# Kernel tuning notes

Measured on AMD Instinct MI355X. Metric: run time of the kernel, lower is better.

The kernel has to match this reference:

```python
import jax, jax.numpy as jnp
import numpy as np

QLEN, MLEN, BSZ = 1024, 1024, 4
D_MODEL, N_HEAD, D_HEAD, D_INNER = 1024, 16, 64, 4096
KLEN = QLEN + MLEN  # = rlen
LN_EPS = 1e-5


def setup_inputs() -> dict:
    key = jax.random.key(0)
    ks = jax.random.split(key, 16)
    s = 0.02
    nhd = N_HEAD * D_HEAD
    inp = {
        "dec_inp": jax.random.normal(ks[0], (QLEN, BSZ, D_MODEL), jnp.float32),
        "r": jax.random.normal(ks[1], (KLEN, D_MODEL), jnp.float32),
        "r_w_bias": jax.random.normal(ks[2], (N_HEAD, D_HEAD), jnp.float32) * s,
        "r_r_bias": jax.random.normal(ks[3], (N_HEAD, D_HEAD), jnp.float32) * s,
        "mems": jax.random.normal(ks[4], (MLEN, BSZ, D_MODEL), jnp.float32),
        # causal mask with memory: position j visible to query i iff j <= i + MLEN
        "dec_attn_mask": (jnp.arange(KLEN)[None, :] > (jnp.arange(QLEN)[:, None] + MLEN))[:, :, None],
        # parameters
        "qkv_w": jax.random.normal(ks[5], (D_MODEL, 3 * nhd), jnp.float32) * s,
        "r_w": jax.random.normal(ks[6], (D_MODEL, nhd), jnp.float32) * s,
        "o_w": jax.random.normal(ks[7], (nhd, D_MODEL), jnp.float32) * s,
        "ln1_w": jnp.ones((D_MODEL,), jnp.float32),
        "ln1_b": jnp.zeros((D_MODEL,), jnp.float32),
        "ln2_w": jnp.ones((D_MODEL,), jnp.float32),
        "ln2_b": jnp.zeros((D_MODEL,), jnp.float32),
        "ff_w1": jax.random.normal(ks[8], (D_MODEL, D_INNER), jnp.float32) * s,
        "ff_b1": jnp.zeros((D_INNER,), jnp.float32),
        "ff_w2": jax.random.normal(ks[9], (D_INNER, D_MODEL), jnp.float32) * s,
        "ff_b2": jnp.zeros((D_MODEL,), jnp.float32),
    }
    return inp


def _layer_norm(x, w, b):
    mu = jnp.mean(x, axis=-1, keepdims=True)
    var = jnp.mean(jnp.square(x - mu), axis=-1, keepdims=True)
    return (x - mu) * jax.lax.rsqrt(var + LN_EPS) * w + b


def _rel_shift(x):
    # x: [qlen, rlen, bsz, n_head] -- Transformer-XL pad/reshape shift
    q, rl = x.shape[0], x.shape[1]
    zero_pad = jnp.zeros((q, 1) + x.shape[2:], x.dtype)
    x_padded = jnp.concatenate([zero_pad, x], axis=1)
    x_padded = x_padded.reshape((rl + 1, q) + x.shape[2:])
    return x_padded[1:].reshape(x.shape)


def reference(dec_inp, r, r_w_bias, r_r_bias, mems, dec_attn_mask,
              qkv_w, r_w, o_w, ln1_w, ln1_b, ln2_w, ln2_b,
              ff_w1, ff_b1, ff_w2, ff_b2):
    qlen, bsz = dec_inp.shape[0], dec_inp.shape[1]
    nhd = N_HEAD * D_HEAD
    scale = 1.0 / (D_HEAD ** 0.5)

    cat = jnp.concatenate([mems, dec_inp], axis=0)          # [klen, b, d]
    w_heads = cat @ qkv_w                                   # [klen, b, 3*nhd]
    w_head_q, w_head_k, w_head_v = jnp.split(w_heads, 3, axis=-1)
    w_head_q = w_head_q[-qlen:]                             # [qlen, b, nhd]
    klen = w_head_k.shape[0]

    w_head_q = w_head_q.reshape(qlen, bsz, N_HEAD, D_HEAD)
    w_head_k = w_head_k.reshape(klen, bsz, N_HEAD, D_HEAD)
    w_head_v = w_head_v.reshape(klen, bsz, N_HEAD, D_HEAD)
    r_head_k = (r @ r_w).reshape(-1, N_HEAD, D_HEAD)        # [rlen, n, d]

    AC = jnp.einsum('ibnd,jbnd->ijbn', w_head_q + r_w_bias, w_head_k)
    BD = jnp.einsum('ibnd,jnd->ijbn', w_head_q + r_r_bias, r_head_k)
    BD = _rel_shift(BD)

    attn_score = (AC + BD) * scale                          # [q, k, b, n]
    attn_score = jnp.where(dec_attn_mask[:, :, :, None], -jnp.inf, attn_score)
    attn_prob = jax.nn.softmax(attn_score, axis=1)

    attn_vec = jnp.einsum('ijbn,jbnd->ibnd', attn_prob, w_head_v)
    attn_out = attn_vec.reshape(qlen, bsz, nhd) @ o_w       # [q, b, d]

    output = _layer_norm(dec_inp + attn_out, ln1_w, ln1_b)
    ff = jax.nn.relu(output @ ff_w1 + ff_b1) @ ff_w2 + ff_b2
    return _layer_norm(output + ff, ln2_w, ln2_b)
```

## Files before the change

### kernel.cpp

```cpp
#include <hip/hip_runtime.h>
#include <hip/hip_bf16.h>
#include <math.h>

#define QLEN 1024
#define MLEN 1024
#define BSZ 4
#define KLEN 2048
#define NH 16
#define DH 64
#define DM 1024
#define DI 4096
#define NHD 1024
#define LN_EPS 1e-5f

typedef short bf16x8 __attribute__((ext_vector_type(8)));
typedef float f32x4 __attribute__((ext_vector_type(4)));
typedef unsigned int uint4v __attribute__((ext_vector_type(4)));

__device__ __forceinline__ float bf2f(unsigned short u) {
    union { unsigned u32; float f; } x; x.u32 = ((unsigned)u) << 16; return x.f;
}
__device__ __forceinline__ unsigned short f2bf(float f) {
    __hip_bfloat16 h = __float2bfloat16(f);
    return *(unsigned short*)&h;
}

static const size_t OFF_CATB  = 0;
static const size_t OFF_VTG   = 0;
static const size_t OFF_WHB   = 16777216;
static const size_t OFF_RB    = 67108864;
static const size_t OFF_RHKB  = 71303168;
static const size_t OFF_AVB   = 75497472;
static const size_t OFF_TMP   = 83886080;
static const size_t OFF_LN1F  = 100663296;
static const size_t OFF_LN1B  = 117440512;
static const size_t OFF_FFHB  = 125829120;
static const size_t OFF_QKVWT = 159383552;
static const size_t OFF_RWT   = 165675008;
static const size_t OFF_OWT   = 167772160;
static const size_t OFF_FFW1T = 169869312;
static const size_t OFF_FFW2T = 178257920;
static const size_t OFF_BK    = 186646528;
static const size_t OFF_BR    = 187170816;

__global__ __launch_bounds__(256) void cast_cat(const float* __restrict__ mems,
                                                const float* __restrict__ dec,
                                                unsigned short* __restrict__ out) {
    size_t i8 = ((size_t)blockIdx.x * 256 + threadIdx.x) * 8;
    const size_t half = (size_t)MLEN * BSZ * DM;
    const float* src = (i8 < half) ? (mems + i8) : (dec + (i8 - half));
    float4 v0 = *(const float4*)src;
    float4 v1 = *(const float4*)(src + 4);
    ushort4 o0 = {f2bf(v0.x), f2bf(v0.y), f2bf(v0.z), f2bf(v0.w)};
    ushort4 o1 = {f2bf(v1.x), f2bf(v1.y), f2bf(v1.z), f2bf(v1.w)};
    *(ushort4*)&out[i8] = o0;
    *(ushort4*)&out[i8 + 4] = o1;
}

__global__ __launch_bounds__(256) void cast_f32_bf16(const float* __restrict__ in,
                                                     unsigned short* __restrict__ out) {
    size_t i8 = ((size_t)blockIdx.x * 256 + threadIdx.x) * 8;
    float4 v0 = *(const float4*)(in + i8);
    float4 v1 = *(const float4*)(in + i8 + 4);
    ushort4 o0 = {f2bf(v0.x), f2bf(v0.y), f2bf(v0.z), f2bf(v0.w)};
    ushort4 o1 = {f2bf(v1.x), f2bf(v1.y), f2bf(v1.z), f2bf(v1.w)};
    *(ushort4*)&out[i8] = o0;
    *(ushort4*)&out[i8 + 4] = o1;
}

__global__ __launch_bounds__(256) void transpose_cast(const float* __restrict__ in,
                                                      unsigned short* __restrict__ out,
                                                      int K, int N) {
    __shared__ float tile[32][33];
    const int t = threadIdx.x;
    const int n0 = blockIdx.x * 32;
    const int k0 = blockIdx.y * 32;
    const int r = t >> 3;
    const int c0 = (t & 7) << 2;
    float4 v = *(const float4*)&in[(size_t)(k0 + r) * N + n0 + c0];
    tile[r][c0 + 0] = v.x; tile[r][c0 + 1] = v.y;
    tile[r][c0 + 2] = v.z; tile[r][c0 + 3] = v.w;
    __syncthreads();
    ushort4 o = {f2bf(tile[c0 + 0][r]), f2bf(tile[c0 + 1][r]),
                 f2bf(tile[c0 + 2][r]), f2bf(tile[c0 + 3][r])};
    *(ushort4*)&out[(size_t)(n0 + r) * K + k0 + c0] = o;
}

__global__ __launch_bounds__(256) void gemm_bf16(const unsigned short* __restrict__ A,
                                                 const unsigned short* __restrict__ Bt,
                                                 const float* __restrict__ bias,
                                                 void* __restrict__ C,
                                                 int M, int N, int K, int flags) {
    __shared__ __align__(16) unsigned short As[128 * 64];
    __shared__ __align__(16) unsigned short Bs[128 * 64];

    const int tid = threadIdx.x;
    const int w = tid >> 6, l = tid & 63;
    const int wr = w >> 1, wc = w & 1;
    const int row0 = blockIdx.y * 128;
    const int col0 = blockIdx.x * 128;

    f32x4 acc[4][4] = {};

    uint4v ra[4], rb[4];
    {
#pragma unroll
        for (int q = 0; q < 4; ++q) {
            int f = q * 256 + tid, r = f >> 3, c = f & 7;
            ra[q] = *(const uint4v*)&A[(size_t)(row0 + r) * K + c * 8];
            rb[q] = *(const uint4v*)&Bt[(size_t)(col0 + r) * K + c * 8];
        }
    }

    const int nt = K >> 6;
    for (int kt = 0; kt < nt; ++kt) {
        __syncthreads();
#pragma unroll
        for (int q = 0; q < 4; ++q) {
            int f = q * 256 + tid, r = f >> 3, c = f & 7;
            int sw = (c ^ (r & 7)) << 3;
            *(uint4v*)&As[r * 64 + sw] = ra[q];
            *(uint4v*)&Bs[r * 64 + sw] = rb[q];
        }
        __syncthreads();
        if (kt + 1 < nt) {
            const int k0 = (kt + 1) << 6;
#pragma unroll
            for (int q = 0; q < 4; ++q) {
                int f = q * 256 + tid, r = f >> 3, c = f & 7;
                ra[q] = *(const uint4v*)&A[(size_t)(row0 + r) * K + k0 + c * 8];
                rb[q] = *(const uint4v*)&Bt[(size_t)(col0 + r) * K + k0 + c * 8];
            }
        }
#pragma unroll
        for (int ks = 0; ks < 2; ++ks) {
            bf16x8 a[4], bfr[4];
#pragma unroll
            for (int m = 0; m < 4; ++m) {
                int arow = wr * 64 + m * 16 + (l & 15);
                int chunk = (ks * 4 + (l >> 4)) ^ (arow & 7);
                a[m] = *(const bf16x8*)&As[arow * 64 + chunk * 8];
            }
#pragma unroll
            for (int n = 0; n < 4; ++n) {
                int brow = wc * 64 + n * 16 + (l & 15);
                int chunk = (ks * 4 + (l >> 4)) ^ (brow & 7);
                bfr[n] = *(const bf16x8*)&Bs[brow * 64 + chunk * 8];
            }
#pragma unroll
            for (int m = 0; m < 4; ++m)
#pragma unroll
                for (int n = 0; n < 4; ++n)
                    acc[m][n] = __builtin_amdgcn_mfma_f32_16x16x32_bf16(a[m], bfr[n], acc[m][n], 0, 0, 0);
        }
    }

#pragma unroll
    for (int n = 0; n < 4; ++n) {
        const int ccol = col0 + wc * 64 + n * 16 + (l & 15);
        const float bv = (flags & 1) ? bias[ccol] : 0.0f;
#pragma unroll
        for (int m = 0; m < 4; ++m) {
            const int crow0 = row0 + wr * 64 + m * 16 + ((l >> 4) << 2);
#pragma unroll
            for (int reg = 0; reg < 4; ++reg) {
                float v = acc[m][n][reg] + bv;
                if (flags & 2) v = fmaxf(v, 0.0f);
                if (flags & 4)
                    ((unsigned short*)C)[(size_t)(crow0 + reg) * N + ccol] = f2bf(v);
                else
                    ((float*)C)[(size_t)(crow0 + reg) * N + ccol] = v;
            }
        }
    }
}

__global__ __launch_bounds__(256) void vtrans(const unsigned short* __restrict__ whb,
                                              unsigned short* __restrict__ vtg) {
    __shared__ unsigned short tile[64][72];
    const int bn = blockIdx.y;
    const int b = bn >> 4, n = bn & 15, nb = n * 64;
    const int jt0 = blockIdx.x * 64;
    const int tid = threadIdx.x;
#pragma unroll
    for (int g = 0; g < 2; ++g) {
        int f = g * 256 + tid;
        int key = f >> 3, c = f & 7;
        uint4v v = *(const uint4v*)&whb[((size_t)(jt0 + key) * 4 + b) * 3072 + 2048 + nb + c * 8];
        *(uint4v*)&tile[key][c * 8] = v;
    }
    __syncthreads();
#pragma unroll
    for (int g = 0; g < 2; ++g) {
        int f = g * 256 + tid;
        int d = f >> 3, ck = f & 7;
        unsigned short tmp[8];
#pragma unroll
        for (int e = 0; e < 8; ++e) tmp[e] = tile[ck * 8 + e][d];
        *(uint4v*)&vtg[(size_t)bn * 131072 + (size_t)d * 2048 + jt0 + ck * 8] = *(uint4v*)tmp;
    }
}

__global__ __launch_bounds__(256) void bias_kernel(const unsigned short* __restrict__ whb,
                                                   const unsigned short* __restrict__ rhkb,
                                                   const float* __restrict__ r_w_bias,
                                                   const float* __restrict__ r_r_bias,
                                                   float* __restrict__ bias_k,
                                                   float* __restrict__ bias_r) {
    int id = blockIdx.x * 256 + threadIdx.x;
    if (id < 64 * 2048) {
        int bn = id >> 11, j = id & 2047;
        int b = bn >> 4, n = bn & 15;
        const unsigned short* kp = &whb[((size_t)j * 4 + b) * 3072 + 1024 + n * 64];
        const float* wb = &r_w_bias[n * 64];
        float acc = 0.f;
#pragma unroll
        for (int d = 0; d < 64; ++d) acc += wb[d] * bf2f(kp[d]);
        bias_k[id] = acc * 0.125f;
    } else {
        int id2 = id - 64 * 2048;
        if (id2 < 16 * 2048) {
            int n = id2 >> 11, rel = id2 & 2047;
            const unsigned short* rp = &rhkb[(size_t)rel * 1024 + n * 64];
            const float* rb = &r_r_bias[n * 64];
            float acc = 0.f;
#pragma unroll
            for (int d = 0; d < 64; ++d) acc += rb[d] * bf2f(rp[d]);
            bias_r[id2] = acc * 0.125f;
        }
    }
}

__global__ __launch_bounds__(512) void flash_attn_mfma(const unsigned short* __restrict__ whb,
                                                       const unsigned short* __restrict__ rhkb,
                                                       const unsigned short* __restrict__ vtg,
                                                       const float* __restrict__ bias_k,
                                                       const float* __restrict__ bias_r,
                                                       unsigned short* __restrict__ avb) {
    const int bid = blockIdx.x;
    const int bn = bid >> 3;
    const int z = bid & 7;
    const int bx = (z & 1) ? (z >> 1) : 7 - (z >> 1);
    const int b = bn >> 4, n = bn & 15, nb = n * 64;
    const int i0 = bx << 7;
    const int tid = threadIdx.x;
    const int wq = tid >> 6;
    const int lane = tid & 63;
    const int rg = lane >> 4;
    const int lc = lane & 15;

    __shared__ __align__(16) unsigned short Ks[4096];
    __shared__ __align__(16) unsigned short Rs[16384];
    __shared__ __align__(16) unsigned short Vt[4096];
    __shared__ __align__(16) unsigned short WS[8][1600];

    bf16x8 qf[2];
    {
        const int qrow = MLEN + i0 + wq * 16 + lc;
        const unsigned short* qp = whb + ((size_t)qrow * 4 + b) * 3072 + nb + rg * 8;
        bf16x8 q0 = *(const bf16x8*)(qp);
        bf16x8 q1 = *(const bf16x8*)(qp + 32);
#pragma unroll
        for (int e = 0; e < 8; ++e) {
            unsigned short u0 = (unsigned short)q0[e];
            unsigned short u1 = (unsigned short)q1[e];
            qf[0][e] = (short)(((u0 & 0x7F80) > 0x0180) ? (unsigned short)(u0 - 0x0180)
                                                        : (unsigned short)(u0 & 0x8000));
            qf[1][e] = (short)(((u1 & 0x7F80) > 0x0180) ? (unsigned short)(u1 - 0x0180)
                                                        : (unsigned short)(u1 & 0x8000));
        }
    }

    f32x4 Oacc[4] = {};
    float mrun[4] = {-INFINITY, -INFINITY, -INFINITY, -INFINITY};
    float lrun[4] = {0.f, 0.f, 0.f, 0.f};

    const int ntiles = 2 * bx + 18;
    const int wbase_off = 112 - 16 * wq;

    const int srow = tid >> 3;
    const int sc = tid & 7;

    uint4v pk, pv, pr3[3];
    {
        pk = *(const uint4v*)&whb[((size_t)srow * 4 + b) * 3072 + 1024 + nb + sc * 8];
        pv = *(const uint4v*)&vtg[(size_t)bn * 131072 + (size_t)srow * 2048 + sc * 8];
        const int relbase0 = 896 - i0;
#pragma unroll
        for (int p = 0; p < 3; ++p) {
            const int a = relbase0 + p * 64 + srow;
            pr3[p] = *(const uint4v*)&rhkb[(size_t)a * 1024 + nb + sc * 8];
        }
    }

    for (int kt = 0; kt < ntiles; ++kt) {
        const int jt0 = kt << 6;
        const int relbase = jt0 - i0 + 896;
        __syncthreads();

        *(uint4v*)&Ks[srow * 64 + ((sc ^ (srow & 7)) << 3)] = pk;
        *(uint4v*)&Vt[srow * 64 + ((sc ^ (srow & 7)) << 3)] = pv;
        if (kt == 0) {
#pragma unroll
            for (int p = 0; p < 3; ++p) {
                const int a = relbase + p * 64 + srow;
                const int dst = ((a >> 6) & 3) * 4096 + (a & 63) * 64 + ((sc ^ (a & 7)) << 3);
                *(uint4v*)&Rs[dst] = pr3[p];
            }
        } else {
            const int a = relbase + 128 + srow;
            const int dst = ((a >> 6) & 3) * 4096 + (a & 63) * 64 + ((sc ^ (a & 7)) << 3);
            *(uint4v*)&Rs[dst] = pr3[0];
        }
        if (kt + 1 < ntiles) {
            const int jn = jt0 + 64;
            pk = *(const uint4v*)&whb[((size_t)(jn + srow) * 4 + b) * 3072 + 1024 + nb + sc * 8];
            pv = *(const uint4v*)&vtg[(size_t)bn * 131072 + (size_t)srow * 2048 + jn + sc * 8];
            int a = relbase + 192 + srow;
            if (a > 2047) a = 2047;
            pr3[0] = *(const uint4v*)&rhkb[(size_t)a * 1024 + nb + sc * 8];
        }
        __syncthreads();

        f32x4 Sacc[4];
        __builtin_amdgcn_s_setprio(1);
#pragma unroll
        for (int nf = 0; nf < 4; ++nf) {
            const int key = nf * 16 + lc;
            const int c7 = key & 7;
            const bf16x8 kf0 = *(const bf16x8*)&Ks[key * 64 + ((rg ^ c7) << 3)];
            const bf16x8 kf1 = *(const bf16x8*)&Ks[key * 64 + (((4 + rg) ^ c7) << 3)];
            f32x4 zz = {0.f, 0.f, 0.f, 0.f};
            zz = __builtin_amdgcn_mfma_f32_16x16x32_bf16(qf[0], kf0, zz, 0, 0, 0);
            Sacc[nf] = __builtin_amdgcn_mfma_f32_16x16x32_bf16(qf[1], kf1, zz, 0, 0, 0);
        }
        __builtin_amdgcn_s_setprio(0);

        unsigned short* bdt = &WS[wq][0];
        const int wbase = relbase + wbase_off;
#pragma unroll
        for (int e5 = 0; e5 < 5; ++e5) {
            const int a = wbase + e5 * 16 + lc;
            const int rbase = ((a >> 6) & 3) * 4096 + (a & 63) * 64;
            const int c7 = a & 7;
            const bf16x8 rf0 = *(const bf16x8*)&Rs[rbase + ((rg ^ c7) << 3)];
            const bf16x8 rf1 = *(const bf16x8*)&Rs[rbase + (((4 + rg) ^ c7) << 3)];
            f32x4 bd = {0.f, 0.f, 0.f, 0.f};
            bd = __builtin_amdgcn_mfma_f32_16x16x32_bf16(qf[0], rf0, bd, 0, 0, 0);
            bd = __builtin_amdgcn_mfma_f32_16x16x32_bf16(qf[1], rf1, bd, 0, 0, 0);
            const int aa = a > 2047 ? 2047 : a;
            const float brv = bias_r[n * 2048 + aa];
            const int bb = e5 * 16 + lc;
            ushort4 p4 = {f2bf(bd[0] + brv), f2bf(bd[1] + brv),
                          f2bf(bd[2] + brv), f2bf(bd[3] + brv)};
            *(ushort4*)&bdt[bb * 20 + rg * 4] = p4;
        }

        float sv[4][4];
        float tmax[4] = {-INFINITY, -INFINITY, -INFINITY, -INFINITY};
#pragma unroll
        for (int nf = 0; nf < 4; ++nf) {
            const int jl = nf * 16 + lc;
            const float bkv = bias_k[(size_t)bn * 2048 + jt0 + jl];
            const int wbb = wbase + 15 + jl;
#pragma unroll
            for (int r = 0; r < 4; ++r) {
                const int qr = rg * 4 + r;
                const int bb = 15 + jl - qr;
                float s = Sacc[nf][r] + bkv + bf2f(bdt[bb * 20 + qr]);
                s = (wbb - qr <= 2047) ? s : -INFINITY;
                sv[nf][r] = s;
                tmax[r] = fmaxf(tmax[r], s);
            }
        }
        float ef[4];
#pragma unroll
        for (int r = 0; r < 4; ++r) {
            float tm = tmax[r];
            tm = fmaxf(tm, __shfl_xor(tm, 1));
            tm = fmaxf(tm, __shfl_xor(tm, 2));
            tm = fmaxf(tm, __shfl_xor(tm, 4));
            tm = fmaxf(tm, __shfl_xor(tm, 8));
            const float mn = fmaxf(mrun[r], tm);
            ef[r] = __expf(mrun[r] - mn);
            mrun[r] = mn;
        }
        float rsum[4] = {0.f, 0.f, 0.f, 0.f};
#pragma unroll
        for (int nf = 0; nf < 4; ++nf) {
            const int jl = nf * 16 + lc;
#pragma unroll
            for (int r = 0; r < 4; ++r) {
                const int qr = rg * 4 + r;
                const float p = __expf(sv[nf][r] - mrun[r]);
                rsum[r] += p;
                bdt[qr * 64 + (((jl >> 3) ^ (qr & 7)) << 3) + (jl & 7)] = f2bf(p);
            }
        }
#pragma unroll
        for (int r = 0; r < 4; ++r) {
            float rs = rsum[r];
            rs += __shfl_xor(rs, 1);
            rs += __shfl_xor(rs, 2);
            rs += __shfl_xor(rs, 4);
            rs += __shfl_xor(rs, 8);
            lrun[r] = lrun[r] * ef[r] + rs;
        }
#pragma unroll
        for (int nf = 0; nf < 4; ++nf)
#pragma unroll
            for (int r = 0; r < 4; ++r) Oacc[nf][r] *= ef[r];

        {
            const int c7 = lc & 7;
            const bf16x8 pf0 = *(const bf16x8*)&bdt[lc * 64 + ((rg ^ c7) << 3)];
            const bf16x8 pf1 = *(const bf16x8*)&bdt[lc * 64 + (((4 + rg) ^ c7) << 3)];
            __builtin_amdgcn_s_setprio(1);
#pragma unroll
            for (int nf = 0; nf < 4; ++nf) {
                const int d = nf * 16 + lc;
                const int d7 = d & 7;
                const bf16x8 vf0 = *(const bf16x8*)&Vt[d * 64 + ((rg ^ d7) << 3)];
                const bf16x8 vf1 = *(const bf16x8*)&Vt[d * 64 + (((4 + rg) ^ d7) << 3)];
                Oacc[nf] = __builtin_amdgcn_mfma_f32_16x16x32_bf16(pf0, vf0, Oacc[nf], 0, 0, 0);
                Oacc[nf] = __builtin_amdgcn_mfma_f32_16x16x32_bf16(pf1, vf1, Oacc[nf], 0, 0, 0);
            }
            __builtin_amdgcn_s_setprio(0);
        }
    }

    float inv[4];
#pragma unroll
    for (int r = 0; r < 4; ++r) inv[r] = 1.0f / lrun[r];
#pragma unroll
    for (int nf = 0; nf < 4; ++nf) {
        const int d = nf * 16 + lc;
#pragma unroll
        for (int r = 0; r < 4; ++r) {
            const int iq = i0 + wq * 16 + rg * 4 + r;
            avb[((size_t)iq * 4 + b) * 1024 + nb + d] = f2bf(Oacc[nf][r] * inv[r]);
        }
    }
}

__global__ __launch_bounds__(256) void add_ln_kernel(const float* __restrict__ a,
                                                     const float* __restrict__ b,
                                                     const float* __restrict__ w,
                                                     const float* __restrict__ bias,
                                                     float* __restrict__ out,
                                                     unsigned short* __restrict__ out_bf) {
    const int row = blockIdx.x;
    const int t = threadIdx.x;
    __shared__ float xs[DM];
    __shared__ float red[256];

    const float* ar = a + (size_t)row * DM;
    const float* br = b + (size_t)row * DM;

    float lsum = 0.f;
#pragma unroll
    for (int c = t; c < DM; c += 256) {
        float v = ar[c] + br[c];
        xs[c] = v;
        lsum += v;
    }
    red[t] = lsum;
    __syncthreads();
    for (int off = 128; off > 0; off >>= 1) {
        if (t < off) red[t] += red[t + off];
        __syncthreads();
    }
    const float mu = red[0] * (1.0f / DM);
    __syncthreads();

    float lvar = 0.f;
#pragma unroll
    for (int c = t; c < DM; c += 256) {
        float dv = xs[c] - mu;
        lvar += dv * dv;
    }
    red[t] = lvar;
    __syncthreads();
    for (int off = 128; off > 0; off >>= 1) {
        if (t < off) red[t] += red[t + off];
        __syncthreads();
    }
    const float rstd = rsqrtf(red[0] * (1.0f / DM) + LN_EPS);
    __syncthreads();

    float* orow = out + (size_t)row * DM;
#pragma unroll
    for (int c = t; c < DM; c += 256) {
        float v = (xs[c] - mu) * rstd * w[c] + bias[c];
        orow[c] = v;
        if (out_bf) out_bf[(size_t)row * DM + c] = f2bf(v);
    }
}

extern "C" void kernel_launch(void* const* d_in, const int* in_sizes, int n_in,
                              void* d_out, int out_size, void* d_ws, size_t ws_size,
                              hipStream_t stream) {
    const float* dec_inp  = (const float*)d_in[0];
    const float* r        = (const float*)d_in[1];
    const float* r_w_bias = (const float*)d_in[2];
    const float* r_r_bias = (const float*)d_in[3];
    const float* mems     = (const float*)d_in[4];
    const float* qkv_w    = (const float*)d_in[6];
    const float* r_w      = (const float*)d_in[7];
    const float* o_w      = (const float*)d_in[8];
    const float* ln1_w    = (const float*)d_in[9];
    const float* ln1_b    = (const float*)d_in[10];
    const float* ln2_w    = (const float*)d_in[11];
    const float* ln2_b    = (const float*)d_in[12];
    const float* ff_w1    = (const float*)d_in[13];
    const float* ff_b1    = (const float*)d_in[14];
    const float* ff_w2    = (const float*)d_in[15];
    const float* ff_b2    = (const float*)d_in[16];
    float* out = (float*)d_out;
    char* ws = (char*)d_ws;

    unsigned short* catb  = (unsigned short*)(ws + OFF_CATB);
    unsigned short* vtg   = (unsigned short*)(ws + OFF_VTG);
    unsigned short* whb   = (unsigned short*)(ws + OFF_WHB);
    unsigned short* rb    = (unsigned short*)(ws + OFF_RB);
    unsigned short* rhkb  = (unsigned short*)(ws + OFF_RHKB);
    unsigned short* avb   = (unsigned short*)(ws + OFF_AVB);
    float*          tmp   = (float*)(ws + OFF_TMP);
    float*          ln1f  = (float*)(ws + OFF_LN1F);
    unsigned short* ln1b  = (unsigned short*)(ws + OFF_LN1B);
    unsigned short* ffhb  = (unsigned short*)(ws + OFF_FFHB);
    unsigned short* qkvwT = (unsigned short*)(ws + OFF_QKVWT);
    unsigned short* rwT   = (unsigned short*)(ws + OFF_RWT);
    unsigned short* owT   = (unsigned short*)(ws + OFF_OWT);
    unsigned short* ffw1T = (unsigned short*)(ws + OFF_FFW1T);
    unsigned short* ffw2T = (unsigned short*)(ws + OFF_FFW2T);
    float*          bk    = (float*)(ws + OFF_BK);
    float*          brr   = (float*)(ws + OFF_BR);

    cast_cat<<<dim3(4096), 256, 0, stream>>>(mems, dec_inp, catb);
    cast_f32_bf16<<<dim3(1024), 256, 0, stream>>>(r, rb);
    transpose_cast<<<dim3(96, 32), 256, 0, stream>>>(qkv_w, qkvwT, 1024, 3072);
    transpose_cast<<<dim3(32, 32), 256, 0, stream>>>(r_w, rwT, 1024, 1024);
    transpose_cast<<<dim3(32, 32), 256, 0, stream>>>(o_w, owT, 1024, 1024);
    transpose_cast<<<dim3(128, 32), 256, 0, stream>>>(ff_w1, ffw1T, 1024, 4096);
    transpose_cast<<<dim3(32, 128), 256, 0, stream>>>(ff_w2, ffw2T, 4096, 1024);

    gemm_bf16<<<dim3(24, 64), 256, 0, stream>>>(catb, qkvwT, nullptr, whb,
                                                KLEN * BSZ, 3 * NHD, DM, 4);
    gemm_bf16<<<dim3(8, 16), 256, 0, stream>>>(rb, rwT, nullptr, rhkb,
                                               KLEN, NHD, DM, 4);

    vtrans<<<dim3(32, 64), 256, 0, stream>>>(whb, vtg);
    bias_kernel<<<dim3(640), 256, 0, stream>>>(whb, rhkb, r_w_bias, r_r_bias, bk, brr);

    flash_attn_mfma<<<dim3(512), 512, 0, stream>>>(
        whb, rhkb, vtg, bk, brr, avb);

    gemm_bf16<<<dim3(8, 32), 256, 0, stream>>>(avb, owT, nullptr, tmp,
                                               QLEN * BSZ, DM, NHD, 0);
    add_ln_kernel<<<dim3(QLEN * BSZ), 256, 0, stream>>>(
        dec_inp, tmp, ln1_w, ln1_b, ln1f, ln1b);
    gemm_bf16<<<dim3(32, 32), 256, 0, stream>>>(ln1b, ffw1T, ff_b1, ffhb,
                                                QLEN * BSZ, DI, DM, 1 | 2 | 4);
    gemm_bf16<<<dim3(8, 32), 256, 0, stream>>>(ffhb, ffw2T, ff_b2, tmp,
                                               QLEN * BSZ, DM, DI, 1);
    add_ln_kernel<<<dim3(QLEN * BSZ), 256, 0, stream>>>(
        ln1f, tmp, ln2_w, ln2_b, out, nullptr);
}
```

Measured before the change: 447.0 us.

## Fuse weight transposes and compute rel-shift BD via lane shuffles in registers

Merges the five weight transpose-cast launches into one kernel that picks its matrix by block index, which removes launch overhead. In the attention kernel the relative-shift BD term is no longer written to a per-wave LDS staging buffer in bf16 and read back. It is now computed per 16-key chunk and realigned with __shfl across lanes, keeping the value in fp32 and shrinking shared memory. It also skips the mask compare on tiles that cannot hit the boundary and skips the O-accumulator rescale when no row max changed, at the cost of extra shuffles and a wave vote.

After: 444.6 us. Within noise of the previous version (-0.5%).

```diff
diff --git a/kernel.cpp b/kernel.cpp
--- a/kernel.cpp
+++ b/kernel.cpp
@@ -68,13 +68,24 @@
     *(ushort4*)&out[i8 + 4] = o1;
 }
 
-__global__ __launch_bounds__(256) void transpose_cast(const float* __restrict__ in,
-                                                      unsigned short* __restrict__ out,
-                                                      int K, int N) {
+__global__ __launch_bounds__(256) void transpose_cast_all(
+        const float* __restrict__ qkv_w, const float* __restrict__ r_w,
+        const float* __restrict__ o_w,  const float* __restrict__ ff_w1,
+        const float* __restrict__ ff_w2,
+        unsigned short* __restrict__ qkvwT, unsigned short* __restrict__ rwT,
+        unsigned short* __restrict__ owT, unsigned short* __restrict__ ffw1T,
+        unsigned short* __restrict__ ffw2T) {
     __shared__ float tile[32][33];
+    const int bid = blockIdx.x;
+    const float* in; unsigned short* out; int K, N, nx, lid;
+    if (bid < 3072)      { in = qkv_w; out = qkvwT; K = 1024; N = 3072; nx = 96;  lid = bid; }
+    else if (bid < 4096) { in = r_w;   out = rwT;   K = 1024; N = 1024; nx = 32;  lid = bid - 3072; }
+    else if (bid < 5120) { in = o_w;   out = owT;   K = 1024; N = 1024; nx = 32;  lid = bid - 4096; }
+    else if (bid < 9216) { in = ff_w1; out = ffw1T; K = 1024; N = 4096; nx = 128; lid = bid - 5120; }
+    else                 { in = ff_w2; out = ffw2T; K = 4096; N = 1024; nx = 32;  lid = bid - 9216; }
+    const int n0 = (lid % nx) * 32;
+    const int k0 = (lid / nx) * 32;
     const int t = threadIdx.x;
-    const int n0 = blockIdx.x * 32;
-    const int k0 = blockIdx.y * 32;
     const int r = t >> 3;
     const int c0 = (t & 7) << 2;
     float4 v = *(const float4*)&in[(size_t)(k0 + r) * N + n0 + c0];
@@ -252,7 +263,7 @@
     __shared__ __align__(16) unsigned short Ks[4096];
     __shared__ __align__(16) unsigned short Rs[16384];
     __shared__ __align__(16) unsigned short Vt[4096];
-    __shared__ __align__(16) unsigned short WS[8][1600];
+    __shared__ __align__(16) unsigned short Ps[8][1024];
 
     bf16x8 qf[2];
     {
@@ -280,6 +291,15 @@
 
     const int srow = tid >> 3;
     const int sc = tid & 7;
+
+    int srcl[4];
+    bool hi5[4];
+#pragma unroll
+    for (int r = 0; r < 4; ++r) {
+        const int qr = rg * 4 + r;
+        srcl[r] = (rg << 4) | ((15 + lc - qr) & 15);
+        hi5[r] = (lc > qr);
+    }
 
     uint4v pk, pv, pr3[3];
     {
@@ -336,11 +356,14 @@
         }
         __builtin_amdgcn_s_setprio(0);
 
-        unsigned short* bdt = &WS[wq][0];
         const int wbase = relbase + wbase_off;
-#pragma unroll
-        for (int e5 = 0; e5 < 5; ++e5) {
-            const int a = wbase + e5 * 16 + lc;
+        const bool needmask = (wbase + 78 > 2047);
+        float sv[4][4];
+        float tmax[4] = {-INFINITY, -INFINITY, -INFINITY, -INFINITY};
+
+        f32x4 bdpA;
+        {
+            const int a = wbase + lc;
             const int rbase = ((a >> 6) & 3) * 4096 + (a & 63) * 64;
             const int c7 = a & 7;
             const bf16x8 rf0 = *(const bf16x8*)&Rs[rbase + ((rg ^ c7) << 3)];
@@ -350,29 +373,44 @@
             bd = __builtin_amdgcn_mfma_f32_16x16x32_bf16(qf[1], rf1, bd, 0, 0, 0);
             const int aa = a > 2047 ? 2047 : a;
             const float brv = bias_r[n * 2048 + aa];
-            const int bb = e5 * 16 + lc;
-            ushort4 p4 = {f2bf(bd[0] + brv), f2bf(bd[1] + brv),
-                          f2bf(bd[2] + brv), f2bf(bd[3] + brv)};
-            *(ushort4*)&bdt[bb * 20 + rg * 4] = p4;
-        }
-
-        float sv[4][4];
-        float tmax[4] = {-INFINITY, -INFINITY, -INFINITY, -INFINITY};
+#pragma unroll
+            for (int r = 0; r < 4; ++r) bdpA[r] = bd[r] + brv;
+        }
 #pragma unroll
         for (int nf = 0; nf < 4; ++nf) {
+            f32x4 bdpB;
+            {
+                const int a = wbase + (nf + 1) * 16 + lc;
+                const int rbase = ((a >> 6) & 3) * 4096 + (a & 63) * 64;
+                const int c7 = a & 7;
+                const bf16x8 rf0 = *(const bf16x8*)&Rs[rbase + ((rg ^ c7) << 3)];
+                const bf16x8 rf1 = *(const bf16x8*)&Rs[rbase + (((4 + rg) ^ c7) << 3)];
+                f32x4 bd = {0.f, 0.f, 0.f, 0.f};
+                bd = __builtin_amdgcn_mfma_f32_16x16x32_bf16(qf[0], rf0, bd, 0, 0, 0);
+                bd = __builtin_amdgcn_mfma_f32_16x16x32_bf16(qf[1], rf1, bd, 0, 0, 0);
+                const int aa = a > 2047 ? 2047 : a;
+                const float brv = bias_r[n * 2048 + aa];
+#pragma unroll
+                for (int r = 0; r < 4; ++r) bdpB[r] = bd[r] + brv;
+            }
             const int jl = nf * 16 + lc;
             const float bkv = bias_k[(size_t)bn * 2048 + jt0 + jl];
-            const int wbb = wbase + 15 + jl;
 #pragma unroll
             for (int r = 0; r < 4; ++r) {
-                const int qr = rg * 4 + r;
-                const int bb = 15 + jl - qr;
-                float s = Sacc[nf][r] + bkv + bf2f(bdt[bb * 20 + qr]);
-                s = (wbb - qr <= 2047) ? s : -INFINITY;
+                const float v0 = __shfl(bdpA[r], srcl[r]);
+                const float v1 = __shfl(bdpB[r], srcl[r]);
+                const float bdv = hi5[r] ? v1 : v0;
+                float s = Sacc[nf][r] + bkv + bdv;
+                if (needmask) {
+                    const int qr = rg * 4 + r;
+                    s = (wbase + 15 + jl - qr <= 2047) ? s : -INFINITY;
+                }
                 sv[nf][r] = s;
                 tmax[r] = fmaxf(tmax[r], s);
             }
-        }
+            bdpA = bdpB;
+        }
+
         float ef[4];
 #pragma unroll
         for (int r = 0; r < 4; ++r) {
@@ -385,6 +423,7 @@
             ef[r] = __expf(mrun[r] - mn);
             mrun[r] = mn;
         }
+        unsigned short* ps = &Ps[wq][0];
         float rsum[4] = {0.f, 0.f, 0.f, 0.f};
 #pragma unroll
         for (int nf = 0; nf < 4; ++nf) {
@@ -394,7 +433,7 @@
                 const int qr = rg * 4 + r;
                 const float p = __expf(sv[nf][r] - mrun[r]);
                 rsum[r] += p;
-                bdt[qr * 64 + (((jl >> 3) ^ (qr & 7)) << 3) + (jl & 7)] = f2bf(p);
+                ps[qr * 64 + (((jl >> 3) ^ (qr & 7)) << 3) + (jl & 7)] = f2bf(p);
             }
         }
 #pragma unroll
@@ -406,15 +445,18 @@
             rs += __shfl_xor(rs, 8);
             lrun[r] = lrun[r] * ef[r] + rs;
         }
-#pragma unroll
-        for (int nf = 0; nf < 4; ++nf)
-#pragma unroll
-            for (int r = 0; r < 4; ++r) Oacc[nf][r] *= ef[r];
+        const int need_rescale = (ef[0] < 1.f) | (ef[1] < 1.f) | (ef[2] < 1.f) | (ef[3] < 1.f);
+        if (__any(need_rescale)) {
+#pragma unroll
+            for (int nf = 0; nf < 4; ++nf)
+#pragma unroll
+                for (int r = 0; r < 4; ++r) Oacc[nf][r] *= ef[r];
+        }
 
         {
             const int c7 = lc & 7;
-            const bf16x8 pf0 = *(const bf16x8*)&bdt[lc * 64 + ((rg ^ c7) << 3)];
-            const bf16x8 pf1 = *(const bf16x8*)&bdt[lc * 64 + (((4 + rg) ^ c7) << 3)];
+            const bf16x8 pf0 = *(const bf16x8*)&ps[lc * 64 + ((rg ^ c7) << 3)];
+            const bf16x8 pf1 = *(const bf16x8*)&ps[lc * 64 + (((4 + rg) ^ c7) << 3)];
             __builtin_amdgcn_s_setprio(1);
 #pragma unroll
             for (int nf = 0; nf < 4; ++nf) {
@@ -539,11 +581,8 @@
 
     cast_cat<<<dim3(4096), 256, 0, stream>>>(mems, dec_inp, catb);
     cast_f32_bf16<<<dim3(1024), 256, 0, stream>>>(r, rb);
-    transpose_cast<<<dim3(96, 32), 256, 0, stream>>>(qkv_w, qkvwT, 1024, 3072);
-    transpose_cast<<<dim3(32, 32), 256, 0, stream>>>(r_w, rwT, 1024, 1024);
-    transpose_cast<<<dim3(32, 32), 256, 0, stream>>>(o_w, owT, 1024, 1024);
-    transpose_cast<<<dim3(128, 32), 256, 0, stream>>>(ff_w1, ffw1T, 1024, 4096);
-    transpose_cast<<<dim3(32, 128), 256, 0, stream>>>(ff_w2, ffw2T, 4096, 1024);
+    transpose_cast_all<<<dim3(13312), 256, 0, stream>>>(
+        qkv_w, r_w, o_w, ff_w1, ff_w2, qkvwT, rwT, owT, ffw1T, ffw2T);
 
     gemm_bf16<<<dim3(24, 64), 256, 0, stream>>>(catb, qkvwT, nullptr, whb,
                                                 KLEN * BSZ, 3 * NHD, DM, 4);
```
